# Optimization experiments

Hardware: AMD Instinct MI355X
Metric: run time of the kernel (lower is better)

Reference implementation:

```python
import jax, jax.numpy as jnp
import numpy as np

E = 8            # num_experts
K = 2            # top-k
CF = 1.25        # capacity_factor
NOISE_STD = 1.0 / E   # noise_mult / num_experts


def setup_inputs() -> dict:
    key = jax.random.key(0)
    ks = jax.random.split(key, 4)
    B, S, D, H = 8, 1024, 768, 3072
    x = jax.random.normal(ks[0], (B, S, D), jnp.float32)
    router_w = jax.random.normal(ks[1], (D, E), jnp.float32) * 0.02
    fc1_w = jax.random.normal(ks[2], (E, D, H), jnp.float32) * 0.02
    fc1_b = jnp.zeros((E, H), jnp.float32)
    fc2_w = jax.random.normal(ks[3], (E, H, D), jnp.float32) * 0.02
    fc2_b = jnp.zeros((E, D), jnp.float32)
    return dict(x=x, router_w=router_w, fc1_w=fc1_w, fc1_b=fc1_b, fc2_w=fc2_w, fc2_b=fc2_b)


def reference(x, router_w, fc1_w, fc1_b, fc2_w, fc2_b):
    B, S, D = x.shape
    N = B * S
    A = N * K                                   # total (token, slot) assignments
    capacity = int(round(K * N * CF / E))
    x_flat = x.reshape(N, D)

    # ---- router (eval mode: no noise, no dropout) ----
    logits = (x_flat @ router_w).astype(jnp.float32)          # [N,E]
    clean_probs = jax.nn.softmax(logits, axis=-1)
    noisy_logits = logits
    noisy_probs = jax.nn.softmax(noisy_logits, axis=-1)
    topk_probs, topk_idx = jax.lax.top_k(noisy_probs, K)      # [N,K]
    topk_probs = topk_probs.astype(x.dtype)

    flat_e = topk_idx.reshape(-1)                             # [A]
    expert_counts = jax.ops.segment_sum(jnp.ones((A,), jnp.float32), flat_e, num_segments=E)

    # ---- aux losses ----
    importance = clean_probs.sum(0)
    mi = importance.mean()
    loss_importance = jnp.var(importance) / (mi * mi + 1e-6)
    # kthvalue(noisy_logits, E-K+1) == (E-K+1)-th smallest == sorted[:, E-K]
    threshold = jnp.sort(noisy_logits, axis=-1)[:, E - K][:, None]
    prob_selected = 1.0 - jax.scipy.stats.norm.cdf(threshold - logits, loc=0.0, scale=NOISE_STD)
    load = prob_selected.sum(0)
    ml = load.mean()
    loss_load = jnp.var(load) / (ml * ml + 1e-6)
    aux_loss = 0.5 * (loss_importance + loss_load)

    # ---- priority-based capacity dropping (vectorized over all assignments) ----
    priority = clean_probs.max(-1)                            # [N]
    tok = jnp.repeat(jnp.arange(N, dtype=jnp.int32), K)       # [A] token of each assignment
    kslot = jnp.tile(jnp.arange(K, dtype=jnp.int32), N)       # [A] which top-k slot
    score = priority[tok] - kslot.astype(jnp.float32)         # combined_scores = -k_idx + priority
    # group by expert (ascending), within expert sort by score descending
    sort_key = flat_e.astype(jnp.float32) * (K + 2) - score
    order = jnp.argsort(sort_key)
    e_sorted = flat_e[order]
    counts = jax.ops.segment_sum(jnp.ones((A,), jnp.int32), flat_e, num_segments=E)
    starts = jnp.cumsum(counts) - counts
    rank_sorted = jnp.arange(A, dtype=jnp.int32) - starts[e_sorted]   # position within expert group
    rank = jnp.zeros((A,), jnp.int32).at[order].set(rank_sorted)
    keep = rank < capacity
    dropped = jnp.sum(~keep).astype(jnp.int32)

    # ---- dispatch into fixed [E, capacity] buffer (overflow slot sliced off) ----
    pos = jnp.where(keep, flat_e * capacity + rank, E * capacity)
    dispatch_tok = jnp.zeros((E * capacity + 1,), jnp.int32).at[pos].set(tok)[:-1]
    w_flat = topk_probs.reshape(-1)
    weight_buf = jnp.zeros((E * capacity + 1,), x.dtype).at[pos].set(jnp.where(keep, w_flat, 0.0))[:-1]

    xe = x_flat[dispatch_tok].reshape(E, capacity, D)         # gather
    h = jax.nn.gelu(jnp.einsum('ecd,edh->ech', xe, fc1_w) + fc1_b[:, None, :], approximate=False)
    ye = jnp.einsum('ech,ehd->ecd', h, fc2_w) + fc2_b[:, None, :]
    weighted = ye * weight_buf.reshape(E, capacity, 1)
    # padded slots have weight 0 and token 0 -> contribute nothing
    out_flat = jnp.zeros((N, D), x.dtype).at[dispatch_tok].add(weighted.reshape(E * capacity, D))

    return out_flat.reshape(B, S, D), aux_loss, dropped, expert_counts
```

## Files before the change

### kernel.cpp

```cpp
#include <hip/hip_runtime.h>
#include <hip/hip_bf16.h>
#include <math.h>

#define NTOK 8192
#define DIM  768
#define HDIM 3072
#define NE   8
#define CAP  2560
#define AMAX 16384

typedef __bf16 bf16x8  __attribute__((ext_vector_type(8)));
typedef __bf16 bf16x4  __attribute__((ext_vector_type(4)));
typedef __bf16 bf16x2  __attribute__((ext_vector_type(2)));
typedef float  floatx4 __attribute__((ext_vector_type(4)));

typedef unsigned int u32_g __attribute__((address_space(1)));
typedef unsigned int u32_l __attribute__((address_space(3)));

__device__ __forceinline__ void gl_lds16(const void* g, void* l) {
  __builtin_amdgcn_global_load_lds((const u32_g*)g, (u32_l*)l, 16, 0, 0);
}

__device__ __forceinline__ float gelu_exact(float v) {
  float z = fabsf(v) * 0.7071067811865475f;
  float t = __builtin_amdgcn_rcpf(1.0f + 0.3275911f * z);
  float p = ((((1.061405429f * t - 1.453152027f) * t + 1.421413741f) * t
              - 0.284496736f) * t + 0.254829592f) * t;
  float e = 1.0f - p * __expf(-z * z);
  e = copysignf(e, v);
  return 0.5f * v * (1.0f + e);
}

__global__ __launch_bounds__(256) void transpose_conv2(
    const float* __restrict__ w1, const float* __restrict__ w2,
    __bf16* __restrict__ o1, __bf16* __restrict__ o2)
{
  const int which = blockIdx.z;
  const float* src = which ? w2 : w1;
  __bf16* dst = which ? o2 : o1;
  const int Kd = which ? HDIM : DIM;
  const int Nd = which ? DIM : HDIM;
  const int e = blockIdx.y;
  const int tilesK = Kd >> 6;
  const int bk = blockIdx.x % tilesK, bn = blockIdx.x / tilesK;
  __shared__ float T[64][65];
  const float* se = src + (size_t)e * Kd * Nd;
  const int k0 = bk * 64, n0 = bn * 64;
  const int tid = threadIdx.x;
#pragma unroll
  for (int it = 0; it < 4; ++it) {
    int flat4 = tid + it * 256;
    int kk = flat4 >> 4, c4 = flat4 & 15;
    float4 v = *(const float4*)(se + (size_t)(k0 + kk) * Nd + n0 + c4 * 4);
    T[kk][c4 * 4 + 0] = v.x; T[kk][c4 * 4 + 1] = v.y;
    T[kk][c4 * 4 + 2] = v.z; T[kk][c4 * 4 + 3] = v.w;
  }
  __syncthreads();
  const int n = tid >> 2, kg = tid & 3;
  bf16x8 v0, v1;
#pragma unroll
  for (int q = 0; q < 8; ++q) v0[q] = (__bf16)T[kg * 16 + q][n];
#pragma unroll
  for (int q = 0; q < 8; ++q) v1[q] = (__bf16)T[kg * 16 + 8 + q][n];
  __bf16* de = dst + (size_t)e * Nd * Kd + (size_t)(n0 + n) * Kd + k0 + kg * 16;
  *(bf16x8*)(de) = v0;
  *(bf16x8*)(de + 8) = v1;
}

__global__ __launch_bounds__(256) void router_kernel(
    const float* __restrict__ x, const float* __restrict__ rw,
    int* __restrict__ list_len, double* __restrict__ imp, double* __restrict__ loadacc,
    int* __restrict__ aidx, float* __restrict__ keyarr, float* __restrict__ warr)
{
  __shared__ float Wl[NE * DIM];
  __shared__ int   lcount[NE], lbase[NE];
  __shared__ int   s_e[32][2], s_pos[32][2];
  __shared__ float s_key[32][2], s_w[32][2];
  const int tid = threadIdx.x;
  for (int i = tid; i < NE * DIM; i += 256) {
    int e = i / DIM, d = i - e * DIM;
    Wl[i] = rw[d * NE + e];
  }
  if (tid < NE) lcount[tid] = 0;
  __syncthreads();
  const int wave = tid >> 6, lane = tid & 63;
  double my_imp = 0.0, my_load = 0.0;

  for (int it = 0; it < 8; ++it) {
    const int t = wave * 8 + it;
    const int n = blockIdx.x * 32 + t;
    const float* xr = x + (size_t)n * DIM;
    float part[NE];
#pragma unroll
    for (int e = 0; e < NE; ++e) part[e] = 0.f;
#pragma unroll
    for (int c = 0; c < DIM / 64; ++c) {
      float xv = xr[c * 64 + lane];
#pragma unroll
      for (int e = 0; e < NE; ++e) part[e] += xv * Wl[e * DIM + c * 64 + lane];
    }
#pragma unroll
    for (int off = 32; off > 0; off >>= 1) {
#pragma unroll
      for (int e = 0; e < NE; ++e) part[e] += __shfl_xor(part[e], off);
    }
    int e0 = 0; float v0 = part[0];
#pragma unroll
    for (int e = 1; e < NE; ++e) if (part[e] > v0) { v0 = part[e]; e0 = e; }
    int e1 = -1; float v1 = -3.4e38f;
#pragma unroll
    for (int e = 0; e < NE; ++e) if (e != e0 && part[e] > v1) { v1 = part[e]; e1 = e; }

    float pexp[NE]; float s = 0.f;
#pragma unroll
    for (int e = 0; e < NE; ++e) { pexp[e] = expf(part[e] - v0); s += pexp[e]; }
    const float inv = 1.0f / s;
    const float pr = inv;
    float w1v = 0.f;
#pragma unroll
    for (int e = 0; e < NE; ++e) if (e == e1) w1v = pexp[e] * inv;

    float myl = 0.f, mypexp = 0.f;
#pragma unroll
    for (int e = 0; e < NE; ++e) if (lane == e) { myl = part[e]; mypexp = pexp[e]; }
    if (lane < NE) {
      my_imp  += (double)(mypexp * inv);
      my_load += (double)(0.5f * erfcf((v1 - myl) * 5.656854249492380f));
    }
    if (lane == 0) {
      int p0 = atomicAdd(&lcount[e0], 1);
      int p1 = atomicAdd(&lcount[e1], 1);
      s_e[t][0] = e0; s_pos[t][0] = p0;
      s_key[t][0] = (float)(e0 * 4) - pr;
      s_w[t][0] = pr;
      s_e[t][1] = e1; s_pos[t][1] = p1;
      s_key[t][1] = (float)(e1 * 4) - (pr - 1.0f);
      s_w[t][1] = w1v;
    }
  }
  __syncthreads();
  if (tid < NE) lbase[tid] = atomicAdd(&list_len[tid], lcount[tid]);
  __syncthreads();
  if (tid < 64) {
    const int t = tid >> 1, sl = tid & 1;
    const int e = s_e[t][sl];
    const int gp = lbase[e] + s_pos[t][sl];
    const int n = blockIdx.x * 32 + t;
    aidx[e * AMAX + gp]   = n * 2 + sl;
    keyarr[e * AMAX + gp] = s_key[t][sl];
    warr[e * AMAX + gp]   = s_w[t][sl];
  }
  if (lane < NE) {
    unsafeAtomicAdd(&imp[lane], my_imp);
    unsafeAtomicAdd(&loadacc[lane], my_load);
  }
}

__global__ __launch_bounds__(256) void compact_kernel(
    const int* __restrict__ list_len, const int* __restrict__ aidx,
    const float* __restrict__ keyarr, const float* __restrict__ warr,
    int* __restrict__ dtok, float* __restrict__ dw,
    const double* __restrict__ imp, const double* __restrict__ loadacc,
    float* __restrict__ out_scalars)
{
  __shared__ float sk[6144];
  __shared__ int   sa[6144];
  const int e = blockIdx.x, tid = threadIdx.x;
  const int C = list_len[e];
  if (C <= CAP) {
    for (int t = tid; t < C; t += 256) {
      int a = aidx[e * AMAX + t];
      dtok[e * CAP + t] = a >> 1;
      dw[e * CAP + t]   = warr[e * AMAX + t];
    }
  } else {
    const bool useL = (C <= 6144);
    if (useL) {
      for (int t = tid; t < C; t += 256) { sk[t] = keyarr[e*AMAX+t]; sa[t] = aidx[e*AMAX+t]; }
      __syncthreads();
    }
    for (int t = tid; t < C; t += 256) {
      float kt = keyarr[e*AMAX+t]; int at = aidx[e*AMAX+t];
      int r = 0;
      for (int u = 0; u < C; ++u) {
        float ku = useL ? sk[u] : keyarr[e*AMAX+u];
        int   au = useL ? sa[u] : aidx[e*AMAX+u];
        if (ku < kt || (ku == kt && au < at)) ++r;
      }
      if (r < CAP) { dtok[e*CAP + r] = at >> 1; dw[e*CAP + r] = warr[e*AMAX+t]; }
    }
  }
  if (e == 0 && tid == 0) {
    double mi = 0, ml = 0;
    for (int i = 0; i < NE; ++i) { mi += imp[i]; ml += loadacc[i]; }
    mi /= NE; ml /= NE;
    double vi = 0, vl = 0;
    for (int i = 0; i < NE; ++i) {
      double di = imp[i] - mi;     vi += di * di;
      double dl = loadacc[i] - ml; vl += dl * dl;
    }
    vi /= NE; vl /= NE;
    double li = vi / (mi * mi + 1e-6), ll = vl / (ml * ml + 1e-6);
    out_scalars[0] = (float)(0.5 * (li + ll));
    int drop = 0;
    for (int i = 0; i < NE; ++i) { int c2 = list_len[i]; if (c2 > CAP) drop += c2 - CAP; }
    out_scalars[1] = (float)drop;
    for (int i = 0; i < NE; ++i) out_scalars[2 + i] = (float)list_len[i];
  }
}

__global__ __launch_bounds__(256) void gather_kernel(
    const float* __restrict__ x, const int* __restrict__ dtok,
    const int* __restrict__ list_len, __bf16* __restrict__ Ag)
{
  const int row  = blockIdx.x * 4 + (threadIdx.x >> 6);
  const int lane = threadIdx.x & 63;
  const int e = row / CAP, slot = row - e * CAP;
  const int kept = min(list_len[e], CAP);
  __bf16* dst = Ag + (size_t)row * DIM;
  if (slot < kept) {
    const float* srcr = x + (size_t)dtok[e * CAP + slot] * DIM;
#pragma unroll
    for (int c = 0; c < DIM / 256; ++c) {
      float4 v = *(const float4*)(srcr + c * 256 + lane * 4);
      bf16x4 o; o[0] = (__bf16)v.x; o[1] = (__bf16)v.y; o[2] = (__bf16)v.z; o[3] = (__bf16)v.w;
      *(bf16x4*)(dst + c * 256 + lane * 4) = o;
    }
  } else {
    bf16x4 z; z[0] = (__bf16)0.f; z[1] = (__bf16)0.f; z[2] = (__bf16)0.f; z[3] = (__bf16)0.f;
#pragma unroll
    for (int c = 0; c < DIM / 256; ++c) *(bf16x4*)(dst + c * 256 + lane * 4) = z;
  }
}

#define BAR() __builtin_amdgcn_s_barrier()

#define ST_A(t, bf) do { \
    gl_lds16(gA0 + (size_t)(t) * 32, &S[bf][(wave * 2 + 0) * 512]); \
    gl_lds16(gA1 + (size_t)(t) * 32, &S[bf][(wave * 2 + 1) * 512]); \
  } while (0)

#define ST_B(t, bf) do { \
    gl_lds16(gB0 + (size_t)(t) * 32, &S[bf][8192 + (wave * 2 + 0) * 512]); \
    gl_lds16(gB1 + (size_t)(t) * 32, &S[bf][8192 + (wave * 2 + 1) * 512]); \
  } while (0)

#define RD_A(half, bf) do { \
    _Pragma("unroll") \
    for (int _m = 0; _m < 4; ++_m) \
      aR[_m] = *(const bf16x8*)&S[bf][(wm * 8 + (half) * 4 + _m) * 512 + lane * 8]; \
  } while (0)

#define RD_B(bf) do { \
    _Pragma("unroll") \
    for (int _n = 0; _n < 4; ++_n) \
      bR[_n] = *(const bf16x8*)&S[bf][8192 + (wn * 4 + _n) * 512 + lane * 8]; \
  } while (0)

#define MM(qm) do { \
    __builtin_amdgcn_s_setprio(1); \
    _Pragma("unroll") \
    for (int _m = 0; _m < 4; ++_m) \
      _Pragma("unroll") \
      for (int _n = 0; _n < 4; ++_n) \
        acc[(qm) * 4 + _m][_n] = __builtin_amdgcn_mfma_f32_16x16x32_bf16( \
            aR[_m], bR[_n], acc[(qm) * 4 + _m][_n], 0, 0, 0); \
    __builtin_amdgcn_s_setprio(0); \
  } while (0)

template<int MODE>
__global__ __launch_bounds__(512, 2) void moe_gemm8(
    const __bf16* __restrict__ Aall, const __bf16* __restrict__ BTall,
    const float* __restrict__ bias, __bf16* __restrict__ Hout,
    float* __restrict__ Out, const int* __restrict__ dtok, const float* __restrict__ dww,
    const int* __restrict__ list_len)
{
  const int Kd = MODE ? HDIM : DIM;
  const int Nd = MODE ? DIM : HDIM;
  const int nT = Kd / 32;
  const int QN = MODE ? 3 : 12;
  const int QTOT = 10 * QN;

  const int e = blockIdx.x & 7;
  const int slot = blockIdx.x >> 3;

  const int kept = min(list_len[e], CAP);
  const int mUsed = (kept + 255) >> 8;

  __shared__ __align__(16) __bf16 S[4][16384];

  const int tid = threadIdx.x, lane = tid & 63, wave = tid >> 6;
  const int wm = wave & 1, wn = wave >> 1;
  const int lr = lane & 15, kq = lane >> 4;
  const int quad = lane >> 4, lcol = lane & 15;

  const __bf16* Abase = Aall + (size_t)e * CAP * Kd;
  const __bf16* Bbase = BTall + (size_t)e * Nd * Kd;

  floatx4 acc[8][4];
  bf16x8 aR[4], bR[4];

  for (int qi = slot; qi < QTOT; qi += 32) {
    const int tm = qi / QN, tn = qi % QN;
    if (tm >= mUsed) continue;
    const int m0 = tm * 256, n0 = tn * 256;

    const __bf16* gA0 = Abase + (size_t)(m0 + (wave * 2 + 0) * 16 + lr) * Kd + kq * 8;
    const __bf16* gA1 = Abase + (size_t)(m0 + (wave * 2 + 1) * 16 + lr) * Kd + kq * 8;
    const __bf16* gB0 = Bbase + (size_t)(n0 + (wave * 2 + 0) * 16 + lr) * Kd + kq * 8;
    const __bf16* gB1 = Bbase + (size_t)(n0 + (wave * 2 + 1) * 16 + lr) * Kd + kq * 8;

#pragma unroll
    for (int i = 0; i < 8; ++i)
#pragma unroll
      for (int j = 0; j < 4; ++j) acc[i][j] = (floatx4)0.f;

    BAR();

    ST_A(0, 0); ST_B(0, 0);
    ST_A(1, 1); ST_B(1, 1);
    ST_A(2, 2); ST_B(2, 2);
    __builtin_amdgcn_s_waitcnt(0x0F78);
    BAR();

#pragma unroll 4
    for (int t = 0; t <= nT - 4; ++t) {
      const int bt = t & 3, bs = (t + 3) & 3;
      RD_A(0, bt); RD_B(bt);
      ST_A(t + 3, bs);
      BAR(); MM(0); BAR();
      RD_A(1, bt);
      ST_B(t + 3, bs);
      __builtin_amdgcn_s_waitcnt(0x0F78);
      BAR(); MM(1); BAR();
    }

    {
      int bt = (nT - 3) & 3;
      RD_A(0, bt); RD_B(bt); BAR(); MM(0); BAR();
      RD_A(1, bt);
      __builtin_amdgcn_s_waitcnt(0x0F74);
      BAR(); MM(1); BAR();

      bt = (nT - 2) & 3;
      RD_A(0, bt); RD_B(bt); BAR(); MM(0); BAR();
      RD_A(1, bt);
      __builtin_amdgcn_s_waitcnt(0x0F70);
      BAR(); MM(1); BAR();

      bt = (nT - 1) & 3;
      RD_A(0, bt); RD_B(bt); MM(0);
      RD_A(1, bt); MM(1);
    }

    float bcol[4];
#pragma unroll
    for (int n = 0; n < 4; ++n)
      bcol[n] = bias[e * Nd + n0 + wn * 64 + n * 16 + lcol];

    if (MODE == 0) {
#pragma unroll
      for (int m = 0; m < 8; ++m) {
#pragma unroll
        for (int r = 0; r < 4; ++r) {
          const int row = m0 + wm * 128 + m * 16 + quad * 4 + r;
          __bf16* hrow = Hout + ((size_t)(e * CAP + row)) * Nd + n0 + wn * 64;
#pragma unroll
          for (int n = 0; n < 4; ++n)
            hrow[n * 16 + lcol] = (__bf16)gelu_exact(acc[m][n][r] + bcol[n]);
        }
      }
    } else {
#pragma unroll
      for (int m = 0; m < 8; ++m) {
#pragma unroll
        for (int r = 0; r < 4; ++r) {
          const int row = m0 + wm * 128 + m * 16 + quad * 4 + r;
          const float w = dww[e * CAP + row];
          if (w != 0.0f) {
            const int tok = dtok[e * CAP + row];
            float* orow = Out + (size_t)tok * DIM + n0 + wn * 64;
#pragma unroll
            for (int n = 0; n < 4; ++n)
              unsafeAtomicAdd(&orow[n * 16 + lcol], w * (acc[m][n][r] + bcol[n]));
          }
        }
      }
    }
  }
}

#undef BAR
#undef ST_A
#undef ST_B
#undef RD_A
#undef RD_B
#undef MM

extern "C" void kernel_launch(void* const* d_in, const int* in_sizes, int n_in,
                              void* d_out, int out_size, void* d_ws, size_t ws_size,
                              hipStream_t stream) {
  (void)in_sizes; (void)n_in; (void)out_size; (void)ws_size;
  const float* x  = (const float*)d_in[0];
  const float* rw = (const float*)d_in[1];
  const float* w1 = (const float*)d_in[2];
  const float* b1 = (const float*)d_in[3];
  const float* w2 = (const float*)d_in[4];
  const float* b2 = (const float*)d_in[5];
  float* out = (float*)d_out;
  char* ws = (char*)d_ws;

  int*    list_len = (int*)(ws + 0);
  double* imp      = (double*)(ws + 64);
  double* loadacc  = (double*)(ws + 128);
  int*    dtok     = (int*)(ws + 256);
  float*  dw       = (float*)(ws + 256 + 81920);
  int*    aidx     = (int*)(ws + 164096);
  float*  keyarr   = (float*)(ws + 164096 + 524288);
  float*  warr     = (float*)(ws + 164096 + 1048576);
  __bf16* W1T      = (__bf16*)(ws + 2097152);
  __bf16* W2T      = (__bf16*)(ws + 2097152 + 37748736);
  __bf16* Ag       = (__bf16*)(ws + 2097152 + 2 * 37748736);
  __bf16* hbuf     = (__bf16*)(ws + 2097152 + 2 * 37748736 + 31457280);

  hipMemsetAsync(d_out, 0, (size_t)NTOK * DIM * sizeof(float), stream);
  hipMemsetAsync(ws, 0, 164096, stream);

  transpose_conv2<<<dim3(576, 8, 2), 256, 0, stream>>>(w1, w2, W1T, W2T);
  router_kernel<<<NTOK / 32, 256, 0, stream>>>(x, rw, list_len, imp, loadacc, aidx, keyarr, warr);
  compact_kernel<<<NE, 256, 0, stream>>>(list_len, aidx, keyarr, warr, dtok, dw, imp, loadacc,
                                         out + (size_t)NTOK * DIM);
  gather_kernel<<<(NE * CAP) / 4, 256, 0, stream>>>(x, dtok, list_len, Ag);
  moe_gemm8<0><<<256, 512, 0, stream>>>(Ag, W1T, b1, hbuf, nullptr, nullptr, nullptr, list_len);
  moe_gemm8<1><<<256, 512, 0, stream>>>(hbuf, W2T, b2, nullptr, out, dtok, dw, list_len);
}
```

Baseline: 544.2 us.

## Prefetch next tile's K-slices during GEMM tail and compact tile ordering

The persistent grouped GEMM loop now enumerates only valid tiles (m-major within each n column) and returns early for blocks with no work, instead of skipping invalid tiles inside a fixed loop. During the last three K-steps of a tile, it issues the global-to-LDS loads for the first three K-slices of the next tile, so the pipeline prologue overlaps the current tile's tail and epilogue. Scheduling barriers pin the order of loads and MFMAs. The gather kernel also switches from float4 to float2 per lane. The risks are extra address arithmetic, the changed tile order affecting L2 reuse, and more complex waitcnt logic.

```diff
diff --git a/kernel.cpp b/kernel.cpp
--- a/kernel.cpp
+++ b/kernel.cpp
@@ -10,7 +10,6 @@
 #define AMAX 16384
 
 typedef __bf16 bf16x8  __attribute__((ext_vector_type(8)));
-typedef __bf16 bf16x4  __attribute__((ext_vector_type(4)));
 typedef __bf16 bf16x2  __attribute__((ext_vector_type(2)));
 typedef float  floatx4 __attribute__((ext_vector_type(4)));
 
@@ -221,28 +220,28 @@
   if (slot < kept) {
     const float* srcr = x + (size_t)dtok[e * CAP + slot] * DIM;
 #pragma unroll
-    for (int c = 0; c < DIM / 256; ++c) {
-      float4 v = *(const float4*)(srcr + c * 256 + lane * 4);
-      bf16x4 o; o[0] = (__bf16)v.x; o[1] = (__bf16)v.y; o[2] = (__bf16)v.z; o[3] = (__bf16)v.w;
-      *(bf16x4*)(dst + c * 256 + lane * 4) = o;
+    for (int c = 0; c < DIM / 128; ++c) {
+      float2 v = *(const float2*)(srcr + c * 128 + lane * 2);
+      bf16x2 o; o[0] = (__bf16)v.x; o[1] = (__bf16)v.y;
+      *(bf16x2*)(dst + c * 128 + lane * 2) = o;
     }
   } else {
-    bf16x4 z; z[0] = (__bf16)0.f; z[1] = (__bf16)0.f; z[2] = (__bf16)0.f; z[3] = (__bf16)0.f;
-#pragma unroll
-    for (int c = 0; c < DIM / 256; ++c) *(bf16x4*)(dst + c * 256 + lane * 4) = z;
+    bf16x2 z; z[0] = (__bf16)0.f; z[1] = (__bf16)0.f;
+#pragma unroll
+    for (int c = 0; c < DIM / 128; ++c) *(bf16x2*)(dst + c * 128 + lane * 2) = z;
   }
 }
 
 #define BAR() __builtin_amdgcn_s_barrier()
 
-#define ST_A(t, bf) do { \
-    gl_lds16(gA0 + (size_t)(t) * 32, &S[bf][(wave * 2 + 0) * 512]); \
-    gl_lds16(gA1 + (size_t)(t) * 32, &S[bf][(wave * 2 + 1) * 512]); \
+#define ST_A2(pA0, pA1, koff, bf) do { \
+    gl_lds16((pA0) + (size_t)(koff), &S[bf][(wave * 2 + 0) * 512]); \
+    gl_lds16((pA1) + (size_t)(koff), &S[bf][(wave * 2 + 1) * 512]); \
   } while (0)
 
-#define ST_B(t, bf) do { \
-    gl_lds16(gB0 + (size_t)(t) * 32, &S[bf][8192 + (wave * 2 + 0) * 512]); \
-    gl_lds16(gB1 + (size_t)(t) * 32, &S[bf][8192 + (wave * 2 + 1) * 512]); \
+#define ST_B2(pB0, pB1, koff, bf) do { \
+    gl_lds16((pB0) + (size_t)(koff), &S[bf][8192 + (wave * 2 + 0) * 512]); \
+    gl_lds16((pB1) + (size_t)(koff), &S[bf][8192 + (wave * 2 + 1) * 512]); \
   } while (0)
 
 #define RD_A(half, bf) do { \
@@ -279,13 +278,16 @@
   const int Nd = MODE ? DIM : HDIM;
   const int nT = Kd / 32;
   const int QN = MODE ? 3 : 12;
-  const int QTOT = 10 * QN;
 
   const int e = blockIdx.x & 7;
   const int slot = blockIdx.x >> 3;
 
   const int kept = min(list_len[e], CAP);
   const int mUsed = (kept + 255) >> 8;
+  const int NV = mUsed * QN;
+
+  int v = slot;
+  if (v >= NV) return;
 
   __shared__ __align__(16) __bf16 S[4][16384];
 
@@ -297,62 +299,75 @@
   const __bf16* Abase = Aall + (size_t)e * CAP * Kd;
   const __bf16* Bbase = BTall + (size_t)e * Nd * Kd;
 
+  auto mOf = [&](int vv) { return vv % mUsed; };
+  auto nOf = [&](int vv) { return vv / mUsed; };
+  auto baseA0 = [&](int vv) {
+    return Abase + (size_t)(mOf(vv) * 256 + (wave * 2 + 0) * 16 + lr) * Kd + kq * 8; };
+  auto baseA1 = [&](int vv) {
+    return Abase + (size_t)(mOf(vv) * 256 + (wave * 2 + 1) * 16 + lr) * Kd + kq * 8; };
+  auto baseB0 = [&](int vv) {
+    return Bbase + (size_t)(nOf(vv) * 256 + (wave * 2 + 0) * 16 + lr) * Kd + kq * 8; };
+  auto baseB1 = [&](int vv) {
+    return Bbase + (size_t)(nOf(vv) * 256 + (wave * 2 + 1) * 16 + lr) * Kd + kq * 8; };
+
+  const __bf16 *cA0 = baseA0(v), *cA1 = baseA1(v), *cB0 = baseB0(v), *cB1 = baseB1(v);
+
   floatx4 acc[8][4];
   bf16x8 aR[4], bR[4];
 
-  for (int qi = slot; qi < QTOT; qi += 32) {
-    const int tm = qi / QN, tn = qi % QN;
-    if (tm >= mUsed) continue;
-    const int m0 = tm * 256, n0 = tn * 256;
-
-    const __bf16* gA0 = Abase + (size_t)(m0 + (wave * 2 + 0) * 16 + lr) * Kd + kq * 8;
-    const __bf16* gA1 = Abase + (size_t)(m0 + (wave * 2 + 1) * 16 + lr) * Kd + kq * 8;
-    const __bf16* gB0 = Bbase + (size_t)(n0 + (wave * 2 + 0) * 16 + lr) * Kd + kq * 8;
-    const __bf16* gB1 = Bbase + (size_t)(n0 + (wave * 2 + 1) * 16 + lr) * Kd + kq * 8;
+  ST_A2(cA0, cA1, 0,  0); ST_B2(cB0, cB1, 0,  0);
+  ST_A2(cA0, cA1, 32, 1); ST_B2(cB0, cB1, 32, 1);
+  ST_A2(cA0, cA1, 64, 2); ST_B2(cB0, cB1, 64, 2);
+  __builtin_amdgcn_s_waitcnt(0x0F78);
+  BAR();
+
+  for (;;) {
+    const int vn = v + 32;
+    const bool hasNext = (vn < NV);
+    const __bf16 *nA0 = cA0, *nA1 = cA1, *nB0 = cB0, *nB1 = cB1;
+    if (hasNext) { nA0 = baseA0(vn); nA1 = baseA1(vn); nB0 = baseB0(vn); nB1 = baseB1(vn); }
 
 #pragma unroll
     for (int i = 0; i < 8; ++i)
 #pragma unroll
       for (int j = 0; j < 4; ++j) acc[i][j] = (floatx4)0.f;
-
-    BAR();
-
-    ST_A(0, 0); ST_B(0, 0);
-    ST_A(1, 1); ST_B(1, 1);
-    ST_A(2, 2); ST_B(2, 2);
-    __builtin_amdgcn_s_waitcnt(0x0F78);
-    BAR();
 
 #pragma unroll 4
     for (int t = 0; t <= nT - 4; ++t) {
       const int bt = t & 3, bs = (t + 3) & 3;
       RD_A(0, bt); RD_B(bt);
-      ST_A(t + 3, bs);
+      ST_A2(cA0, cA1, (t + 3) * 32, bs);
+      __builtin_amdgcn_sched_barrier(0);
       BAR(); MM(0); BAR();
       RD_A(1, bt);
-      ST_B(t + 3, bs);
+      ST_B2(cB0, cB1, (t + 3) * 32, bs);
       __builtin_amdgcn_s_waitcnt(0x0F78);
+      __builtin_amdgcn_sched_barrier(0);
       BAR(); MM(1); BAR();
     }
 
-    {
-      int bt = (nT - 3) & 3;
-      RD_A(0, bt); RD_B(bt); BAR(); MM(0); BAR();
+#pragma unroll
+    for (int j = 0; j < 3; ++j) {
+      const int t = nT - 3 + j;
+      const int bt = t & 3, bs = j & 3;
+      RD_A(0, bt); RD_B(bt);
+      if (hasNext) ST_A2(nA0, nA1, j * 32, bs);
+      __builtin_amdgcn_sched_barrier(0);
+      BAR(); MM(0); BAR();
       RD_A(1, bt);
-      __builtin_amdgcn_s_waitcnt(0x0F74);
+      if (hasNext) {
+        ST_B2(nB0, nB1, j * 32, bs);
+        __builtin_amdgcn_s_waitcnt(0x0F78);
+      } else if (j == 0) {
+        __builtin_amdgcn_s_waitcnt(0x0F74);
+      } else if (j == 1) {
+        __builtin_amdgcn_s_waitcnt(0x0F70);
+      }
+      __builtin_amdgcn_sched_barrier(0);
       BAR(); MM(1); BAR();
-
-      bt = (nT - 2) & 3;
-      RD_A(0, bt); RD_B(bt); BAR(); MM(0); BAR();
-      RD_A(1, bt);
-      __builtin_amdgcn_s_waitcnt(0x0F70);
-      BAR(); MM(1); BAR();
-
-      bt = (nT - 1) & 3;
-      RD_A(0, bt); RD_B(bt); MM(0);
-      RD_A(1, bt); MM(1);
-    }
-
+    }
+
+    const int m0 = mOf(v) * 256, n0 = nOf(v) * 256;
     float bcol[4];
 #pragma unroll
     for (int n = 0; n < 4; ++n)
@@ -387,12 +402,15 @@
         }
       }
     }
+
+    if (!hasNext) break;
+    v = vn; cA0 = nA0; cA1 = nA1; cB0 = nB0; cB1 = nB1;
   }
 }
 
 #undef BAR
-#undef ST_A
-#undef ST_B
+#undef ST_A2
+#undef ST_B2
 #undef RD_A
 #undef RD_B
 #undef MM
```

After: 568.1 us. +4.4%, slower.
